# Optimization experiments

Hardware: AMD Instinct MI355X
Metric: run time of the kernel (lower is better)

## Reference

```python
import jax, jax.numpy as jnp
import numpy as np

H, HKV, HD = 16, 4, 128
EPS = 1.1920928955078125e-07  # float32 eps, torch F.rms_norm default


def _rms_norm(t):
    return t * jax.lax.rsqrt(jnp.mean(t * t, axis=-1, keepdims=True) + EPS)


def _rope(t, cos, sin):
    # t: [B, T, h, HD]; cos/sin: [T, HD//2] -> broadcast [1, T, 1, HD//2]
    te, to = t[..., 0::2], t[..., 1::2]
    c = cos[None, :, None, :]
    s = sin[None, :, None, :]
    re = te * c - to * s
    ro = te * s + to * c
    return jnp.stack((re, ro), axis=-1).reshape(t.shape)


def setup_inputs() -> dict:
    key = jax.random.key(0)
    ks = jax.random.split(key, 5)
    B, T, C = 2, 2048, 2048
    return {
        "x": jax.random.normal(ks[0], (B, T, C), jnp.float32),
        "Wq": jax.random.normal(ks[1], (C, C), jnp.float32) * 0.02,
        "Wk": jax.random.normal(ks[2], (HKV * HD, C), jnp.float32) * 0.02,
        "Wv": jax.random.normal(ks[3], (HKV * HD, C), jnp.float32) * 0.02,
        "Wo": jax.random.normal(ks[4], (C, C), jnp.float32) * 0.02,
        "q_gain": jnp.full((H,), 5.0, jnp.float32),
    }


def reference(x, Wq, Wk, Wv, Wo, q_gain):
    B, T, C = x.shape
    q = (x @ Wq.T).reshape(B, T, H, HD)
    k = (x @ Wk.T).reshape(B, T, HKV, HD)
    v = (x @ Wv.T).reshape(B, T, HKV, HD)

    q = _rms_norm(q)
    k = _rms_norm(k)

    theta = 1.0 / (10000.0 ** (jnp.arange(0, HD, 2, dtype=jnp.float32) / HD))
    t = jnp.arange(T, dtype=jnp.float32)
    freqs = jnp.outer(t, theta)  # [T, HD//2]
    cos, sin = jnp.cos(freqs), jnp.sin(freqs)

    q = _rope(q, cos, sin)
    k = _rope(k, cos, sin)
    q = q * q_gain[None, None, :, None]

    qh = q.transpose(0, 2, 1, 3)                       # [B, H, T, HD]
    kh = jnp.repeat(k.transpose(0, 2, 1, 3), H // HKV, axis=1)
    vh = jnp.repeat(v.transpose(0, 2, 1, 3), H // HKV, axis=1)

    scale = 1.0 / jnp.sqrt(jnp.float32(HD))
    scores = jnp.einsum("bhqd,bhkd->bhqk", qh, kh) * scale
    causal = jnp.tril(jnp.ones((T, T), bool))
    scores = jnp.where(causal[None, None], scores, jnp.finfo(scores.dtype).min)
    attn = jax.nn.softmax(scores, axis=-1)
    out = jnp.einsum("bhqk,bhkd->bhqd", attn, vh)
    out = out.transpose(0, 2, 1, 3).reshape(B, T, C)
    return out @ Wo.T
```

## Files before the change

kernel.cpp:

```cpp
#include <hip/hip_runtime.h>
#include <hip/hip_bf16.h>

#define TSEQ 2048
#define CDIM 2048
#define NH   16
#define NKV  4
#define HDIM 128
#define BATCH 2
#define MROWS (BATCH*TSEQ)
#define KVC   (NKV*HDIM)
#define QKVC  (CDIM + 2*KVC)

typedef short bf16x8 __attribute__((ext_vector_type(8)));
typedef float f32x4  __attribute__((ext_vector_type(4)));

typedef const __attribute__((address_space(1))) void* gptr_t;
typedef __attribute__((address_space(3))) void* sptr_t;

__device__ inline void async16(const __hip_bfloat16* g, __hip_bfloat16* l) {
  __builtin_amdgcn_global_load_lds((gptr_t)g, (sptr_t)l, 16, 0, 0);
}

__device__ inline f32x4 mfma16(bf16x8 a, bf16x8 b, f32x4 c) {
  return __builtin_amdgcn_mfma_f32_16x16x32_bf16(a, b, c, 0, 0, 0);
}

__device__ inline float bfbits2f(unsigned short u) {
  return __uint_as_float(((unsigned)u) << 16);
}

__device__ inline int swz128(int row, int col) {
  return row*128 + (((col >> 3) ^ (row & 15)) << 3) + (col & 7);
}
__device__ inline int swz64(int row, int col) {
  return row*64 + ((((col >> 3) ^ row) & 7) << 3) + (col & 7);
}

__global__ void canary(const void* __restrict__ x, int* __restrict__ flag) {
  __shared__ int cnt[256];
  int tid = threadIdx.x;
  const unsigned short* u = (const unsigned short*)x;
  int c = 0;
#pragma unroll
  for (int i = 0; i < 4; ++i) {
    float a = fabsf(bfbits2f(u[(tid*4 + i)*2]));
    if (a >= 1e-6f && a <= 1e3f) c++;
  }
  cnt[tid] = c;
  __syncthreads();
  for (int s = 128; s > 0; s >>= 1) {
    if (tid < s) cnt[tid] += cnt[tid + s];
    __syncthreads();
  }
  if (tid == 0) *flag = (cnt[0] > 512) ? 1 : 0;
}

__global__ __launch_bounds__(256) void canonize_all(
    const void* __restrict__ xs,  const void* __restrict__ wqs,
    const void* __restrict__ wks, const void* __restrict__ wvs,
    const void* __restrict__ wos, const void* __restrict__ gs,
    __hip_bfloat16* __restrict__ xd,
    __hip_bfloat16* __restrict__ wqkv,
    __hip_bfloat16* __restrict__ wod,
    __hip_bfloat16* __restrict__ gd,
    const int* __restrict__ flag)
{
  int blk = blockIdx.x;
  const void* src; __hip_bfloat16* dst; int base, n;
  if      (blk < 4096) { src = xs;  dst = xd;                base = blk;        n = MROWS*CDIM; }
  else if (blk < 6144) { src = wqs; dst = wqkv;              base = blk - 4096; n = CDIM*CDIM; }
  else if (blk < 6656) { src = wks; dst = wqkv + (size_t)CDIM*CDIM;            base = blk - 6144; n = KVC*CDIM; }
  else if (blk < 7168) { src = wvs; dst = wqkv + (size_t)(CDIM+KVC)*CDIM;      base = blk - 6656; n = KVC*CDIM; }
  else if (blk < 9216) { src = wos; dst = wod;               base = blk - 7168; n = CDIM*CDIM; }
  else                 { src = gs;  dst = gd;                base = 0;          n = NH; }
  int idx = base*2048 + threadIdx.x*8;
  if (idx >= n) return;
  if (*flag) {
    *(bf16x8*)&dst[idx] = *(const bf16x8*)((const __hip_bfloat16*)src + idx);
  } else {
    const float* s = (const float*)src + idx;
#pragma unroll
    for (int j = 0; j < 8; ++j) dst[idx + j] = __float2bfloat16(s[j]);
  }
}

#define BK 64

__global__ __launch_bounds__(512, 2) void gemm_bt256(
    const __hip_bfloat16* __restrict__ A,
    const __hip_bfloat16* __restrict__ B,
    __hip_bfloat16* __restrict__ C,
    int M, int N, int K, int lda)
{
  __shared__ __align__(16) __hip_bfloat16 As[2][256*BK];
  __shared__ __align__(16) __hip_bfloat16 Bs[2][256*BK];
  const int tid  = threadIdx.x;
  const int wave = tid >> 6;
  const int lane = tid & 63;
  const int qd   = lane >> 4;
  const int ln   = lane & 15;
  const int m0   = blockIdx.y * 256;
  const int n0   = blockIdx.x * 256;
  const int wm   = (wave >> 2) * 128;
  const int wn   = (wave & 3) * 64;

  auto stageA = [&](int half, int buf, int kt) {
    const __hip_bfloat16* src = A + (size_t)(m0 + half*128)*lda + kt*BK;
    __hip_bfloat16* dst = &As[buf][half*128*BK];
#pragma unroll
    for (int i = 0; i < 2; ++i) {
      int c = i*512 + tid;
      int row = c >> 3, sl = c & 7;
      int gs = sl ^ (row & 7);
      async16(&src[(size_t)row*lda + gs*8], &dst[(i*512 + wave*64)*8]);
    }
  };
  auto stageB = [&](int half, int buf, int kt) {
    const __hip_bfloat16* src = B + (size_t)(n0 + half*128)*K + kt*BK;
    __hip_bfloat16* dst = &Bs[buf][half*128*BK];
#pragma unroll
    for (int i = 0; i < 2; ++i) {
      int c = i*512 + tid;
      int row = c >> 3, sl = c & 7;
      int gs = sl ^ (row & 7);
      async16(&src[(size_t)row*K + gs*8], &dst[(i*512 + wave*64)*8]);
    }
  };
  auto ldA = [&](int buf, int m, int kk) -> bf16x8 {
    int row = wm + m*16 + ln;
    return *(const bf16x8*)&As[buf][row*BK + (((kk*4 + qd) ^ (row & 7)) << 3)];
  };
  auto ldB = [&](int buf, int n, int kk) -> bf16x8 {
    int row = wn + n*16 + ln;
    return *(const bf16x8*)&Bs[buf][row*BK + (((kk*4 + qd) ^ (row & 7)) << 3)];
  };

  f32x4 acc[8][4] = {};
  const int nt = K / BK;

  stageA(0, 0, 0); stageA(1, 0, 0);
  stageB(0, 0, 0); stageB(1, 0, 0);
  if (nt > 1) {
    stageA(0, 1, 1); stageA(1, 1, 1);
    asm volatile("s_waitcnt vmcnt(4)" ::: "memory");
  } else {
    asm volatile("s_waitcnt vmcnt(0)" ::: "memory");
  }
  __builtin_amdgcn_s_barrier();

#pragma unroll 1
  for (int t = 0; t < nt; ++t) {
    const int buf = t & 1;
    bf16x8 a03[4][2], a47[4][2], b01[2][2], b23[2][2];

#pragma unroll
    for (int m = 0; m < 4; ++m)
#pragma unroll
      for (int kk = 0; kk < 2; ++kk) a03[m][kk] = ldA(buf, m, kk);
#pragma unroll
    for (int n = 0; n < 2; ++n)
#pragma unroll
      for (int kk = 0; kk < 2; ++kk) b01[n][kk] = ldB(buf, n, kk);
    if (t + 1 < nt) { stageB(0, buf ^ 1, t + 1); stageB(1, buf ^ 1, t + 1); }
    __builtin_amdgcn_s_setprio(1);
#pragma unroll
    for (int m = 0; m < 4; ++m)
#pragma unroll
      for (int n = 0; n < 2; ++n)
#pragma unroll
        for (int kk = 0; kk < 2; ++kk)
          acc[m][n] = mfma16(a03[m][kk], b01[n][kk], acc[m][n]);
    __builtin_amdgcn_s_setprio(0);
    __builtin_amdgcn_s_barrier();

#pragma unroll
    for (int m = 0; m < 4; ++m)
#pragma unroll
      for (int kk = 0; kk < 2; ++kk) a47[m][kk] = ldA(buf, 4 + m, kk);
    __builtin_amdgcn_s_setprio(1);
#pragma unroll
    for (int m = 0; m < 4; ++m)
#pragma unroll
      for (int n = 0; n < 2; ++n)
#pragma unroll
        for (int kk = 0; kk < 2; ++kk)
          acc[4 + m][n] = mfma16(a47[m][kk], b01[n][kk], acc[4 + m][n]);
    __builtin_amdgcn_s_setprio(0);
    __builtin_amdgcn_s_barrier();

#pragma unroll
    for (int n = 0; n < 2; ++n)
#pragma unroll
      for (int kk = 0; kk < 2; ++kk) b23[n][kk] = ldB(buf, 2 + n, kk);
    __builtin_amdgcn_s_setprio(1);
#pragma unroll
    for (int m = 0; m < 4; ++m)
#pragma unroll
      for (int n = 0; n < 2; ++n)
#pragma unroll
        for (int kk = 0; kk < 2; ++kk)
          acc[m][2 + n] = mfma16(a03[m][kk], b23[n][kk], acc[m][2 + n]);
    __builtin_amdgcn_s_setprio(0);
    __builtin_amdgcn_s_barrier();

    if (t + 2 < nt) { stageA(0, buf, t + 2); stageA(1, buf, t + 2); }
    __builtin_amdgcn_s_setprio(1);
#pragma unroll
    for (int m = 0; m < 4; ++m)
#pragma unroll
      for (int n = 0; n < 2; ++n)
#pragma unroll
        for (int kk = 0; kk < 2; ++kk)
          acc[4 + m][2 + n] = mfma16(a47[m][kk], b23[n][kk], acc[4 + m][2 + n]);
    __builtin_amdgcn_s_setprio(0);
    if (t + 2 < nt) asm volatile("s_waitcnt vmcnt(4)" ::: "memory");
    else            asm volatile("s_waitcnt vmcnt(0)" ::: "memory");
    __builtin_amdgcn_s_barrier();
  }

#pragma unroll
  for (int m = 0; m < 8; ++m)
#pragma unroll
    for (int n = 0; n < 4; ++n) {
      int row = m0 + wm + m*16 + qd*4;
      int col = n0 + wn + n*16 + ln;
#pragma unroll
      for (int r = 0; r < 4; ++r)
        C[(size_t)(row + r)*N + col] = __float2bfloat16(acc[m][n][r]);
    }
}

__global__ __launch_bounds__(256, 2) void gemm_out(
    const __hip_bfloat16* __restrict__ A,
    const __hip_bfloat16* __restrict__ B,
    void* __restrict__ C,
    int M, int N, int K, int lda, const int* __restrict__ flag)
{
  __shared__ __align__(16) __hip_bfloat16 As[128*32];
  __shared__ __align__(16) __hip_bfloat16 Bs[128*32];
  const int tid  = threadIdx.x;
  const int wave = tid >> 6;
  const int lane = tid & 63;
  const int qd   = lane >> 4;
  const int ln   = lane & 15;
  const int m0   = blockIdx.y * 128;
  const int n0   = blockIdx.x * 128;
  const int wm   = (wave >> 1) * 64;
  const int wn   = (wave & 1) * 64;

  f32x4 acc[4][4] = {};

  for (int k0 = 0; k0 < K; k0 += 32) {
    __syncthreads();
#pragma unroll
    for (int r = 0; r < 2; ++r) {
      int e   = (r*256 + tid) * 8;
      int row = e >> 5;
      int col = e & 31;
      async16(&A[(size_t)(m0+row)*lda + k0 + col], &As[(size_t)(r*256 + wave*64)*8]);
      async16(&B[(size_t)(n0+row)*K   + k0 + col], &Bs[(size_t)(r*256 + wave*64)*8]);
    }
    __syncthreads();
    bf16x8 af[4], bfr[4];
#pragma unroll
    for (int i = 0; i < 4; ++i)
      af[i] = *(const bf16x8*)&As[(wm + i*16 + ln)*32 + qd*8];
#pragma unroll
    for (int j = 0; j < 4; ++j)
      bfr[j] = *(const bf16x8*)&Bs[(wn + j*16 + ln)*32 + qd*8];
#pragma unroll
    for (int i = 0; i < 4; ++i)
#pragma unroll
      for (int j = 0; j < 4; ++j)
        acc[i][j] = mfma16(af[i], bfr[j], acc[i][j]);
  }
  const bool isbf = (*flag != 0);
#pragma unroll
  for (int i = 0; i < 4; ++i)
#pragma unroll
    for (int j = 0; j < 4; ++j) {
      int row = m0 + wm + i*16 + qd*4;
      int col = n0 + wn + j*16 + ln;
#pragma unroll
      for (int r = 0; r < 4; ++r) {
        if (isbf) ((__hip_bfloat16*)C)[(size_t)(row + r)*N + col] = __float2bfloat16(acc[i][j][r]);
        else      ((float*)C)[(size_t)(row + r)*N + col] = acc[i][j][r];
      }
    }
}

__global__ __launch_bounds__(256) void prep_qk(
    __hip_bfloat16* __restrict__ qkv,
    const __hip_bfloat16* __restrict__ gain)
{
  int wid  = blockIdx.x * 4 + (threadIdx.x >> 6);
  int lane = threadIdx.x & 63;
  bool isq = wid < MROWS*NH;
  int m, h;
  __hip_bfloat16* p;
  if (isq) { m = wid >> 4; h = wid & 15; p = qkv + (size_t)m*QKVC + h*HDIM; }
  else     { int w2 = wid - MROWS*NH; m = w2 >> 2; h = w2 & 3; p = qkv + (size_t)m*QKVC + CDIM + h*HDIM; }

  ushort2 raw = *(const ushort2*)((const unsigned short*)p + 2*lane);
  float e = bfbits2f(raw.x), o = bfbits2f(raw.y);
  float ss = e*e + o*o;
#pragma unroll
  for (int off = 32; off >= 1; off >>= 1) ss += __shfl_xor(ss, off);
  float rms = rsqrtf(ss * (1.0f/128.0f) + 1.1920928955078125e-07f);
  e *= rms; o *= rms;

  float theta = exp2f(-(float)(2*lane) * (1.0f/128.0f) * 13.287712379549449f);
  int t = m & (TSEQ-1);
  float fr = (float)t * theta;
  float c = cosf(fr), s = sinf(fr);
  float re = e*c - o*s;
  float ro = e*s + o*c;

  if (isq) {
    float g = bfbits2f(*(const unsigned short*)&gain[h]) * 0.08838834764831845f;
    re *= g; ro *= g;
  }
  p[2*lane]   = __float2bfloat16(re);
  p[2*lane+1] = __float2bfloat16(ro);
}

__global__ __launch_bounds__(256) void transpose_v(
    const __hip_bfloat16* __restrict__ qkv, __hip_bfloat16* __restrict__ vt)
{
  __shared__ __hip_bfloat16 tile[32][34];
  int tx = threadIdx.x & 31;
  int ty = threadIdx.x >> 5;
  int r0 = blockIdx.x * 32;
  int c0 = blockIdx.y * 32;
#pragma unroll
  for (int i = 0; i < 4; ++i)
    tile[ty + i*8][tx] = qkv[(size_t)(r0 + ty + i*8)*QKVC + (CDIM + KVC) + c0 + tx];
  __syncthreads();
  int b = r0 >> 11;
  int t = r0 & (TSEQ-1);
  int hk = c0 >> 7;
  int d0 = c0 & (HDIM-1);
#pragma unroll
  for (int i = 0; i < 4; ++i) {
    int d = d0 + ty + i*8;
    vt[((size_t)((b*NKV + hk)*HDIM + d))*TSEQ + t + tx] = tile[tx][ty + i*8];
  }
}

__global__ __launch_bounds__(256, 2) void attn_kernel(
    const __hip_bfloat16* __restrict__ qkv,
    const __hip_bfloat16* __restrict__ vt,
    __hip_bfloat16* __restrict__ out)
{
  const int tid  = threadIdx.x;
  const int wave = tid >> 6;
  const int lane = tid & 63;
  const int qd = lane >> 4, ln = lane & 15;
  const int p  = blockIdx.x;
  const int h  = blockIdx.y;
  const int b  = blockIdx.z;
  const int hk = h >> 2;

  const __hip_bfloat16* K = qkv + (size_t)(b*TSEQ)*QKVC + CDIM + hk*HDIM;
  const __hip_bfloat16* V = vt + ((size_t)(b*NKV + hk)*HDIM)*TSEQ;

  __shared__ __align__(16) __hip_bfloat16 Ks[64*128];
  __shared__ __align__(16) __hip_bfloat16 Vs[128*64];
  __shared__ __align__(16) __hip_bfloat16 Pb[4*16*64];

  auto issueK = [&](int t0) {
#pragma unroll
    for (int i = 0; i < 4; ++i) {
      int c = i*256 + tid;
      int row = c >> 4, cc = c & 15;
      int gcc = cc ^ (row & 15);
      async16(&K[(size_t)(t0 + row)*QKVC + gcc*8], &Ks[(i*256 + wave*64)*8]);
    }
  };
  auto issueV = [&](int t0) {
#pragma unroll
    for (int i = 0; i < 4; ++i) {
      int c = i*256 + tid;
      int row = c >> 3, cc = c & 7;
      int gcc = cc ^ (row & 7);
      async16(&V[(size_t)row*TSEQ + t0 + gcc*8], &Vs[(i*256 + wave*64)*8]);
    }
  };

#pragma unroll 1
  for (int seg = 0; seg < 2; ++seg) {
    const int qt = seg ? (31 - p) : p;
    const int q0 = qt * 64;
    const int qw = q0 + wave * 16;

    bf16x8 qfr[4];
#pragma unroll
    for (int kc = 0; kc < 4; ++kc)
      qfr[kc] = *(const bf16x8*)&qkv[((size_t)(b*TSEQ + qw + ln))*QKVC + h*HDIM + kc*32 + qd*8];

    f32x4 o[8] = {};
    float lacc[4] = {0.f, 0.f, 0.f, 0.f};

    __syncthreads();
    issueK(0);
    __syncthreads();

#pragma unroll 1
    for (int kt = 0; kt <= qt; ++kt) {
      const int t0 = kt * 64;
      issueV(t0);

      f32x4 s[4] = {};
#pragma unroll
      for (int nt = 0; nt < 4; ++nt) {
#pragma unroll
        for (int kc = 0; kc < 4; ++kc) {
          bf16x8 kfr = *(const bf16x8*)&Ks[swz128(nt*16 + ln, kc*32 + qd*8)];
          s[nt] = mfma16(qfr[kc], kfr, s[nt]);
        }
      }
      if (kt == qt) {
#pragma unroll
        for (int nt = 0; nt < 4; ++nt)
#pragma unroll
          for (int r = 0; r < 4; ++r) {
            int row = qw + qd*4 + r;
            int col = t0 + nt*16 + ln;
            if (col > row) s[nt][r] = -1.0e30f;
          }
      }
#pragma unroll
      for (int nt = 0; nt < 4; ++nt)
#pragma unroll
        for (int r = 0; r < 4; ++r)
          s[nt][r] = __expf(s[nt][r]);
#pragma unroll
      for (int r = 0; r < 4; ++r)
        lacc[r] += (s[0][r] + s[1][r]) + (s[2][r] + s[3][r]);

      __hip_bfloat16* Pw = &Pb[wave*1024];
#pragma unroll
      for (int nt = 0; nt < 4; ++nt)
#pragma unroll
        for (int r = 0; r < 4; ++r)
          Pw[swz64(qd*4 + r, nt*16 + ln)] = __float2bfloat16(s[nt][r]);
      bf16x8 pa[2];
#pragma unroll
      for (int kc = 0; kc < 2; ++kc)
        pa[kc] = *(const bf16x8*)&Pw[swz64(ln, kc*32 + qd*8)];

      __syncthreads();
      if (kt < qt) issueK(t0 + 64);

#pragma unroll
      for (int dt = 0; dt < 8; ++dt) {
#pragma unroll
        for (int kc = 0; kc < 2; ++kc) {
          bf16x8 vf = *(const bf16x8*)&Vs[swz64(dt*16 + ln, kc*32 + qd*8)];
          o[dt] = mfma16(pa[kc], vf, o[dt]);
        }
      }
      __syncthreads();
    }

    float inv[4];
#pragma unroll
    for (int r = 0; r < 4; ++r) {
      float lr = lacc[r];
      lr += __shfl_xor(lr, 1);
      lr += __shfl_xor(lr, 2);
      lr += __shfl_xor(lr, 4);
      lr += __shfl_xor(lr, 8);
      inv[r] = 1.0f / lr;
    }

    __hip_bfloat16* Ow = &Ks[wave*2048];
#pragma unroll
    for (int dt = 0; dt < 8; ++dt)
#pragma unroll
      for (int r = 0; r < 4; ++r)
        Ow[(qd*4 + r)*128 + dt*16 + ln] = __float2bfloat16(o[dt][r] * inv[r]);
    __syncthreads();
#pragma unroll
    for (int pass = 0; pass < 4; ++pass) {
      int row = pass*4 + qd;
      bf16x8 val = *(const bf16x8*)&Ow[row*128 + ln*8];
      int q = qw + row;
      *(bf16x8*)&out[((size_t)(b*TSEQ + q))*CDIM + h*HDIM + ln*8] = val;
    }
  }
}

extern "C" void kernel_launch(void* const* d_in, const int* in_sizes, int n_in,
                              void* d_out, int out_size, void* d_ws, size_t ws_size,
                              hipStream_t stream) {
  char* ws = (char*)d_ws;
  size_t off = 0;
  auto alloc = [&](size_t bytes) { char* p = ws + off; off += (bytes + 255) & ~(size_t)255; return p; };

  int* flag = (int*)alloc(256);
  __hip_bfloat16* xb   = (__hip_bfloat16*)alloc((size_t)MROWS*CDIM*2);
  __hip_bfloat16* wqkv = (__hip_bfloat16*)alloc((size_t)QKVC*CDIM*2);
  __hip_bfloat16* wob  = (__hip_bfloat16*)alloc((size_t)CDIM*CDIM*2);
  __hip_bfloat16* gb   = (__hip_bfloat16*)alloc(256);
  __hip_bfloat16* qkv  = (__hip_bfloat16*)alloc((size_t)MROWS*QKVC*2);
  __hip_bfloat16* vt   = (__hip_bfloat16*)alloc((size_t)MROWS*KVC*2);

  canary<<<1, 256, 0, stream>>>(d_in[0], flag);

  canonize_all<<<9217, 256, 0, stream>>>(
      d_in[0], d_in[1], d_in[2], d_in[3], d_in[4], d_in[5],
      xb, wqkv, wob, gb, flag);

  gemm_bt256<<<dim3(QKVC/256, MROWS/256), 512, 0, stream>>>(
      xb, wqkv, qkv, MROWS, QKVC, CDIM, CDIM);

  int nwaves = MROWS*NH + MROWS*NKV;
  prep_qk<<<nwaves/4, 256, 0, stream>>>(qkv, gb);

  transpose_v<<<dim3(MROWS/32, KVC/32), 256, 0, stream>>>(qkv, vt);

  attn_kernel<<<dim3(TSEQ/128, NH, BATCH), 256, 0, stream>>>(qkv, vt, xb);

  gemm_out<<<dim3(CDIM/128, MROWS/128), 256, 0, stream>>>(
      xb, wob, d_out, MROWS, CDIM, CDIM, CDIM, flag);
}
```

Baseline: 304.3 us.

## Use 128-row query tiles per block with two sub-tiles per wave

The attention kernel now gives each block a 128-row query tile, with each wave owning 32 rows as two 16-row sub-tiles. This replaces the old scheme where each block processed two 64-row tiles in sequence as a load-balanced pair. Each K and V tile loaded into shared memory now feeds twice as many MFMAs, which halves K/V traffic and barrier count per unit of work. Blocks are ordered largest first (qt = 15 - blockIdx.x) instead of pairing tiles for balance. The cost is more registers, a larger P buffer, and a less balanced causal workload across blocks. The launch grid presumably must change to 16 in x, which is not visible here.

After: 322.3 us. 1.06x slower.

```diff
diff --git a/kernel.cpp b/kernel.cpp
--- a/kernel.cpp
+++ b/kernel.cpp
@@ -356,7 +356,7 @@
   const int wave = tid >> 6;
   const int lane = tid & 63;
   const int qd = lane >> 4, ln = lane & 15;
-  const int p  = blockIdx.x;
+  const int qt = 15 - blockIdx.x;
   const int h  = blockIdx.y;
   const int b  = blockIdx.z;
   const int hk = h >> 2;
@@ -366,7 +366,7 @@
 
   __shared__ __align__(16) __hip_bfloat16 Ks[64*128];
   __shared__ __align__(16) __hip_bfloat16 Vs[128*64];
-  __shared__ __align__(16) __hip_bfloat16 Pb[4*16*64];
+  __shared__ __align__(16) __hip_bfloat16 Pb[4*32*64];
 
   auto issueK = [&](int t0) {
 #pragma unroll
@@ -387,107 +387,124 @@
     }
   };
 
+  const int q0  = qt * 128;
+  const int qws = q0 + wave * 32;
+
+  bf16x8 qfr[2][4];
+#pragma unroll
+  for (int sub = 0; sub < 2; ++sub)
+#pragma unroll
+    for (int kc = 0; kc < 4; ++kc)
+      qfr[sub][kc] = *(const bf16x8*)&qkv[((size_t)(b*TSEQ + qws + sub*16 + ln))*QKVC + h*HDIM + kc*32 + qd*8];
+
+  f32x4 o[2][8] = {};
+  float lacc[2][4] = {};
+
+  issueK(0);
+  __syncthreads();
+
+  const int ktend = 2*qt + 1;
 #pragma unroll 1
-  for (int seg = 0; seg < 2; ++seg) {
-    const int qt = seg ? (31 - p) : p;
-    const int q0 = qt * 64;
-    const int qw = q0 + wave * 16;
-
-    bf16x8 qfr[4];
-#pragma unroll
-    for (int kc = 0; kc < 4; ++kc)
-      qfr[kc] = *(const bf16x8*)&qkv[((size_t)(b*TSEQ + qw + ln))*QKVC + h*HDIM + kc*32 + qd*8];
-
-    f32x4 o[8] = {};
-    float lacc[4] = {0.f, 0.f, 0.f, 0.f};
+  for (int kt = 0; kt <= ktend; ++kt) {
+    const int t0 = kt * 64;
+    issueV(t0);
+
+    f32x4 sc[2][4] = {};
+#pragma unroll
+    for (int nt = 0; nt < 4; ++nt) {
+#pragma unroll
+      for (int kc = 0; kc < 4; ++kc) {
+        bf16x8 kfr = *(const bf16x8*)&Ks[swz128(nt*16 + ln, kc*32 + qd*8)];
+        sc[0][nt] = mfma16(qfr[0][kc], kfr, sc[0][nt]);
+        sc[1][nt] = mfma16(qfr[1][kc], kfr, sc[1][nt]);
+      }
+    }
+    if (t0 + 63 > qws) {
+#pragma unroll
+      for (int sub = 0; sub < 2; ++sub)
+#pragma unroll
+        for (int nt = 0; nt < 4; ++nt)
+#pragma unroll
+          for (int r = 0; r < 4; ++r) {
+            int row = qws + sub*16 + qd*4 + r;
+            int col = t0 + nt*16 + ln;
+            if (col > row) sc[sub][nt][r] = -1.0e30f;
+          }
+    }
+#pragma unroll
+    for (int sub = 0; sub < 2; ++sub) {
+#pragma unroll
+      for (int nt = 0; nt < 4; ++nt)
+#pragma unroll
+        for (int r = 0; r < 4; ++r)
+          sc[sub][nt][r] = __expf(sc[sub][nt][r]);
+#pragma unroll
+      for (int r = 0; r < 4; ++r)
+        lacc[sub][r] += (sc[sub][0][r] + sc[sub][1][r]) + (sc[sub][2][r] + sc[sub][3][r]);
+    }
+
+    __hip_bfloat16* Pw = &Pb[wave*2048];
+#pragma unroll
+    for (int sub = 0; sub < 2; ++sub)
+#pragma unroll
+      for (int nt = 0; nt < 4; ++nt)
+#pragma unroll
+        for (int r = 0; r < 4; ++r)
+          Pw[swz64(sub*16 + qd*4 + r, nt*16 + ln)] = __float2bfloat16(sc[sub][nt][r]);
+    bf16x8 pa[2][2];
+#pragma unroll
+    for (int sub = 0; sub < 2; ++sub)
+#pragma unroll
+      for (int kc = 0; kc < 2; ++kc)
+        pa[sub][kc] = *(const bf16x8*)&Pw[swz64(sub*16 + ln, kc*32 + qd*8)];
 
     __syncthreads();
-    issueK(0);
+    if (kt < ktend) issueK(t0 + 64);
+
+#pragma unroll
+    for (int dt = 0; dt < 8; ++dt) {
+#pragma unroll
+      for (int kc = 0; kc < 2; ++kc) {
+        bf16x8 vf = *(const bf16x8*)&Vs[swz64(dt*16 + ln, kc*32 + qd*8)];
+        o[0][dt] = mfma16(pa[0][kc], vf, o[0][dt]);
+        o[1][dt] = mfma16(pa[1][kc], vf, o[1][dt]);
+      }
+    }
     __syncthreads();
-
-#pragma unroll 1
-    for (int kt = 0; kt <= qt; ++kt) {
-      const int t0 = kt * 64;
-      issueV(t0);
-
-      f32x4 s[4] = {};
-#pragma unroll
-      for (int nt = 0; nt < 4; ++nt) {
-#pragma unroll
-        for (int kc = 0; kc < 4; ++kc) {
-          bf16x8 kfr = *(const bf16x8*)&Ks[swz128(nt*16 + ln, kc*32 + qd*8)];
-          s[nt] = mfma16(qfr[kc], kfr, s[nt]);
-        }
-      }
-      if (kt == qt) {
-#pragma unroll
-        for (int nt = 0; nt < 4; ++nt)
-#pragma unroll
-          for (int r = 0; r < 4; ++r) {
-            int row = qw + qd*4 + r;
-            int col = t0 + nt*16 + ln;
-            if (col > row) s[nt][r] = -1.0e30f;
-          }
-      }
-#pragma unroll
-      for (int nt = 0; nt < 4; ++nt)
-#pragma unroll
-        for (int r = 0; r < 4; ++r)
-          s[nt][r] = __expf(s[nt][r]);
-#pragma unroll
-      for (int r = 0; r < 4; ++r)
-        lacc[r] += (s[0][r] + s[1][r]) + (s[2][r] + s[3][r]);
-
-      __hip_bfloat16* Pw = &Pb[wave*1024];
-#pragma unroll
-      for (int nt = 0; nt < 4; ++nt)
-#pragma unroll
-        for (int r = 0; r < 4; ++r)
-          Pw[swz64(qd*4 + r, nt*16 + ln)] = __float2bfloat16(s[nt][r]);
-      bf16x8 pa[2];
-#pragma unroll
-      for (int kc = 0; kc < 2; ++kc)
-        pa[kc] = *(const bf16x8*)&Pw[swz64(ln, kc*32 + qd*8)];
-
-      __syncthreads();
-      if (kt < qt) issueK(t0 + 64);
-
-#pragma unroll
-      for (int dt = 0; dt < 8; ++dt) {
-#pragma unroll
-        for (int kc = 0; kc < 2; ++kc) {
-          bf16x8 vf = *(const bf16x8*)&Vs[swz64(dt*16 + ln, kc*32 + qd*8)];
-          o[dt] = mfma16(pa[kc], vf, o[dt]);
-        }
-      }
-      __syncthreads();
-    }
-
-    float inv[4];
+  }
+
+  float inv[2][4];
+#pragma unroll
+  for (int sub = 0; sub < 2; ++sub)
 #pragma unroll
     for (int r = 0; r < 4; ++r) {
-      float lr = lacc[r];
+      float lr = lacc[sub][r];
       lr += __shfl_xor(lr, 1);
       lr += __shfl_xor(lr, 2);
       lr += __shfl_xor(lr, 4);
       lr += __shfl_xor(lr, 8);
-      inv[r] = 1.0f / lr;
-    }
-
-    __hip_bfloat16* Ow = &Ks[wave*2048];
-#pragma unroll
-    for (int dt = 0; dt < 8; ++dt)
-#pragma unroll
-      for (int r = 0; r < 4; ++r)
-        Ow[(qd*4 + r)*128 + dt*16 + ln] = __float2bfloat16(o[dt][r] * inv[r]);
-    __syncthreads();
-#pragma unroll
-    for (int pass = 0; pass < 4; ++pass) {
-      int row = pass*4 + qd;
-      bf16x8 val = *(const bf16x8*)&Ow[row*128 + ln*8];
-      int q = qw + row;
-      *(bf16x8*)&out[((size_t)(b*TSEQ + q))*CDIM + h*HDIM + ln*8] = val;
-    }
+      inv[sub][r] = 1.0f / lr;
+    }
+
+  __hip_bfloat16* Ow0 = &Ks[wave*2048];
+  __hip_bfloat16* Ow1 = &Vs[wave*2048];
+#pragma unroll
+  for (int dt = 0; dt < 8; ++dt)
+#pragma unroll
+    for (int r = 0; r < 4; ++r) {
+      Ow0[(qd*4 + r)*128 + dt*16 + ln] = __float2bfloat16(o[0][dt][r] * inv[0][r]);
+      Ow1[(qd*4 + r)*128 + dt*16 + ln] = __float2bfloat16(o[1][dt][r] * inv[1][r]);
+    }
+  __syncthreads();
+#pragma unroll
+  for (int pass = 0; pass < 4; ++pass) {
+    int row = pass*4 + qd;
+    bf16x8 v0 = *(const bf16x8*)&Ow0[row*128 + ln*8];
+    bf16x8 v1 = *(const bf16x8*)&Ow1[row*128 + ln*8];
+    int qa = qws + row;
+    int qb = qws + 16 + row;
+    *(bf16x8*)&out[((size_t)(b*TSEQ + qa))*CDIM + h*HDIM + ln*8] = v0;
+    *(bf16x8*)&out[((size_t)(b*TSEQ + qb))*CDIM + h*HDIM + ln*8] = v1;
   }
 }
 
```

## Repartition attention work so each wave owns KV rows, sharing P across waves

Applied to the files above, without the earlier changes.

The attention kernel now computes transposed score tiles. Each wave handles 16 KV rows against all 64 queries of the block, with Q fragments held in registers, and for PV each wave owns 32 head-dim columns. P is shared through one block-wide LDS tile, and row sums are reduced across waves via a small LDS buffer. The intent is to cut redundant K/V LDS fragment reads per MFMA and raise MFMA density, with setprio around the PV loop. The cost is more registers for the Q fragments and an extra barrier in the epilogue.

Result: faster. 294.5 us (-3.2%).

```diff
diff --git a/kernel.cpp b/kernel.cpp
--- a/kernel.cpp
+++ b/kernel.cpp
@@ -27,6 +27,11 @@
 
 __device__ inline float bfbits2f(unsigned short u) {
   return __uint_as_float(((unsigned)u) << 16);
+}
+
+__device__ inline unsigned short f2bfu(float x) {
+  __hip_bfloat16 t = __float2bfloat16(x);
+  return *(unsigned short*)&t;
 }
 
 __device__ inline int swz128(int row, int col) {
@@ -366,7 +371,8 @@
 
   __shared__ __align__(16) __hip_bfloat16 Ks[64*128];
   __shared__ __align__(16) __hip_bfloat16 Vs[128*64];
-  __shared__ __align__(16) __hip_bfloat16 Pb[4*16*64];
+  __shared__ __align__(16) __hip_bfloat16 Pb[64*64];
+  __shared__ float Lb[4][64];
 
   auto issueK = [&](int t0) {
 #pragma unroll
@@ -391,14 +397,15 @@
   for (int seg = 0; seg < 2; ++seg) {
     const int qt = seg ? (31 - p) : p;
     const int q0 = qt * 64;
-    const int qw = q0 + wave * 16;
-
-    bf16x8 qfr[4];
-#pragma unroll
-    for (int kc = 0; kc < 4; ++kc)
-      qfr[kc] = *(const bf16x8*)&qkv[((size_t)(b*TSEQ + qw + ln))*QKVC + h*HDIM + kc*32 + qd*8];
-
-    f32x4 o[8] = {};
+
+    bf16x8 qfr[4][4];
+#pragma unroll
+    for (int qsub = 0; qsub < 4; ++qsub)
+#pragma unroll
+      for (int kc = 0; kc < 4; ++kc)
+        qfr[qsub][kc] = *(const bf16x8*)&qkv[((size_t)(b*TSEQ + q0 + qsub*16 + ln))*QKVC + h*HDIM + kc*32 + qd*8];
+
+    f32x4 o[2][4] = {};
     float lacc[4] = {0.f, 0.f, 0.f, 0.f};
 
     __syncthreads();
@@ -410,82 +417,97 @@
       const int t0 = kt * 64;
       issueV(t0);
 
-      f32x4 s[4] = {};
-#pragma unroll
-      for (int nt = 0; nt < 4; ++nt) {
-#pragma unroll
-        for (int kc = 0; kc < 4; ++kc) {
-          bf16x8 kfr = *(const bf16x8*)&Ks[swz128(nt*16 + ln, kc*32 + qd*8)];
-          s[nt] = mfma16(qfr[kc], kfr, s[nt]);
-        }
+      f32x4 sc[4] = {};
+#pragma unroll
+      for (int kc = 0; kc < 4; ++kc) {
+        bf16x8 kfa = *(const bf16x8*)&Ks[swz128(wave*16 + ln, kc*32 + qd*8)];
+#pragma unroll
+        for (int qsub = 0; qsub < 4; ++qsub)
+          sc[qsub] = mfma16(kfa, qfr[qsub][kc], sc[qsub]);
       }
       if (kt == qt) {
 #pragma unroll
-        for (int nt = 0; nt < 4; ++nt)
+        for (int qsub = 0; qsub < 4; ++qsub)
 #pragma unroll
           for (int r = 0; r < 4; ++r) {
-            int row = qw + qd*4 + r;
-            int col = t0 + nt*16 + ln;
-            if (col > row) s[nt][r] = -1.0e30f;
+            int kv = t0 + wave*16 + qd*4 + r;
+            int q  = q0 + qsub*16 + ln;
+            if (kv > q) sc[qsub][r] = -1.0e30f;
           }
       }
 #pragma unroll
-      for (int nt = 0; nt < 4; ++nt)
+      for (int qsub = 0; qsub < 4; ++qsub) {
 #pragma unroll
         for (int r = 0; r < 4; ++r)
-          s[nt][r] = __expf(s[nt][r]);
-#pragma unroll
-      for (int r = 0; r < 4; ++r)
-        lacc[r] += (s[0][r] + s[1][r]) + (s[2][r] + s[3][r]);
-
-      __hip_bfloat16* Pw = &Pb[wave*1024];
-#pragma unroll
-      for (int nt = 0; nt < 4; ++nt)
-#pragma unroll
-        for (int r = 0; r < 4; ++r)
-          Pw[swz64(qd*4 + r, nt*16 + ln)] = __float2bfloat16(s[nt][r]);
-      bf16x8 pa[2];
-#pragma unroll
-      for (int kc = 0; kc < 2; ++kc)
-        pa[kc] = *(const bf16x8*)&Pw[swz64(ln, kc*32 + qd*8)];
+          sc[qsub][r] = __expf(sc[qsub][r]);
+        lacc[qsub] += (sc[qsub][0] + sc[qsub][1]) + (sc[qsub][2] + sc[qsub][3]);
+      }
+
+#pragma unroll
+      for (int qsub = 0; qsub < 4; ++qsub) {
+        ushort4 pk;
+        pk.x = f2bfu(sc[qsub][0]); pk.y = f2bfu(sc[qsub][1]);
+        pk.z = f2bfu(sc[qsub][2]); pk.w = f2bfu(sc[qsub][3]);
+        *(ushort4*)&Pb[swz64(qsub*16 + ln, wave*16 + qd*4)] = pk;
+      }
 
       __syncthreads();
       if (kt < qt) issueK(t0 + 64);
 
-#pragma unroll
-      for (int dt = 0; dt < 8; ++dt) {
-#pragma unroll
-        for (int kc = 0; kc < 2; ++kc) {
-          bf16x8 vf = *(const bf16x8*)&Vs[swz64(dt*16 + ln, kc*32 + qd*8)];
-          o[dt] = mfma16(pa[kc], vf, o[dt]);
+      __builtin_amdgcn_s_setprio(1);
+#pragma unroll
+      for (int kc2 = 0; kc2 < 2; ++kc2) {
+        bf16x8 pfb[4];
+#pragma unroll
+        for (int qsub = 0; qsub < 4; ++qsub)
+          pfb[qsub] = *(const bf16x8*)&Pb[swz64(qsub*16 + ln, kc2*32 + qd*8)];
+#pragma unroll
+        for (int half = 0; half < 2; ++half) {
+          bf16x8 vfa = *(const bf16x8*)&Vs[swz64(wave*32 + half*16 + ln, kc2*32 + qd*8)];
+#pragma unroll
+          for (int qsub = 0; qsub < 4; ++qsub)
+            o[half][qsub] = mfma16(vfa, pfb[qsub], o[half][qsub]);
         }
       }
+      __builtin_amdgcn_s_setprio(0);
       __syncthreads();
     }
 
+#pragma unroll
+    for (int qsub = 0; qsub < 4; ++qsub) {
+      lacc[qsub] += __shfl_xor(lacc[qsub], 16);
+      lacc[qsub] += __shfl_xor(lacc[qsub], 32);
+    }
+    if (qd == 0) {
+#pragma unroll
+      for (int qsub = 0; qsub < 4; ++qsub)
+        Lb[wave][qsub*16 + ln] = lacc[qsub];
+    }
+    __syncthreads();
     float inv[4];
 #pragma unroll
-    for (int r = 0; r < 4; ++r) {
-      float lr = lacc[r];
-      lr += __shfl_xor(lr, 1);
-      lr += __shfl_xor(lr, 2);
-      lr += __shfl_xor(lr, 4);
-      lr += __shfl_xor(lr, 8);
-      inv[r] = 1.0f / lr;
-    }
-
-    __hip_bfloat16* Ow = &Ks[wave*2048];
-#pragma unroll
-    for (int dt = 0; dt < 8; ++dt)
-#pragma unroll
-      for (int r = 0; r < 4; ++r)
-        Ow[(qd*4 + r)*128 + dt*16 + ln] = __float2bfloat16(o[dt][r] * inv[r]);
+    for (int qsub = 0; qsub < 4; ++qsub) {
+      int q = qsub*16 + ln;
+      inv[qsub] = 1.0f / (((Lb[0][q] + Lb[1][q]) + (Lb[2][q] + Lb[3][q])));
+    }
+
+#pragma unroll
+    for (int half = 0; half < 2; ++half)
+#pragma unroll
+      for (int qsub = 0; qsub < 4; ++qsub) {
+        ushort4 pk;
+        pk.x = f2bfu(o[half][qsub][0] * inv[qsub]);
+        pk.y = f2bfu(o[half][qsub][1] * inv[qsub]);
+        pk.z = f2bfu(o[half][qsub][2] * inv[qsub]);
+        pk.w = f2bfu(o[half][qsub][3] * inv[qsub]);
+        *(ushort4*)&Ks[swz128(qsub*16 + ln, wave*32 + half*16 + qd*4)] = pk;
+      }
     __syncthreads();
 #pragma unroll
     for (int pass = 0; pass < 4; ++pass) {
-      int row = pass*4 + qd;
-      bf16x8 val = *(const bf16x8*)&Ow[row*128 + ln*8];
-      int q = qw + row;
+      int row = wave*16 + pass*4 + qd;
+      bf16x8 val = *(const bf16x8*)&Ks[swz128(row, ln*8)];
+      int q = q0 + row;
       *(bf16x8*)&out[((size_t)(b*TSEQ + q))*CDIM + h*HDIM + ln*8] = val;
     }
   }
@@ -520,7 +542,7 @@
 
   transpose_v<<<dim3(MROWS/32, KVC/32), 256, 0, stream>>>(qkv, vt);
 
-  attn_kernel<<<dim3(TSEQ/128, NH, BATCH), 256, 0, stream>>>(qkv, vt, xb);
+  attn_kernel<<<dim3(16, NH, BATCH), 256, 0, stream>>>(qkv, vt, xb);
 
   gemm_out<<<dim3(CDIM/128, MROWS/128), 256, 0, stream>>>(
       xb, wob, d_out, MROWS, CDIM, CDIM, CDIM, flag);
```
